# Performance work log

Hardware: AMD Instinct MI355X
Metric: run time of the kernel (lower is better)

Reference implementation:

```python
import jax, jax.numpy as jnp
import numpy as np

SHRINK_THRES = 0.0025
R_THRES = 1.0
EPS = 1e-12


def setup_inputs() -> dict:
    key = jax.random.key(0)
    k1, k2 = jax.random.split(key)
    N, L, D = 16384, 4096, 1024  # samples, memory slots (lan_dim), fea_dim
    x = jax.random.normal(k1, (N, D), dtype=jnp.float32)
    stdv = 1.0 / np.sqrt(D)
    weight = jax.random.uniform(k2, (L, D), dtype=jnp.float32, minval=-stdv, maxval=stdv)
    return {"x": x, "weight": weight}


def reference(x, weight):
    # memory addressing: att = softmax(x @ W^T)  -> [N, L]
    att = jax.nn.softmax(x @ weight.T, axis=1)
    # hard_shrink_relu: relu(a - lambd) * a / (|a - lambd| + eps)
    shifted = att - SHRINK_THRES
    att = jax.nn.relu(shifted) * att / (jnp.abs(shifted) + EPS)
    # L1 normalize along dim 1 (F.normalize p=1, eps=1e-12)
    l1 = jnp.sum(jnp.abs(att), axis=1, keepdims=True)
    att = att / jnp.maximum(l1, EPS)
    # reconstruct from memory: [N, D]
    output = att @ weight
    # nearest landmark per sample (detached gather in original)
    ind = jnp.argmax(att, axis=1)                      # [N]
    nl = weight[ind]                                   # [N, D]
    # second-nearest: overwrite argmax slot with the row minimum, re-argmax
    rows = jnp.arange(att.shape[0])
    row_min = jnp.min(att, axis=1)
    att2 = att.at[rows, ind].set(row_min)
    ind2 = jnp.argmax(att2, axis=1)
    nl2 = weight[ind2]                                 # [N, D]
    # centroid-distance filter (original returns list of indices; we return a
    # jit-compatible boolean mask over samples instead)
    cen = jnp.mean(weight, axis=0)                     # [D]
    dist = jnp.sqrt(jnp.sum((x - cen) ** 2, axis=1))   # [N]
    col_mask = dist < R_THRES                          # [N] bool
    return (output, att, nl, nl2, col_mask)
```

## Files before the change

### kernel.cpp

```cpp
#include <hip/hip_runtime.h>
#include <cmath>

#define NS 16384
#define LS 4096
#define DF 1024
#define SHRINK_T 0.0025f
#define EPS_T 1e-12f

using f16 = _Float16;
using f16x8 = __attribute__((ext_vector_type(8))) _Float16;
using f32x16 = __attribute__((ext_vector_type(16))) float;

#define NSEG 64
#define BM 128
#define BN 128
#define BK 32
#define NKT (DF / BK)

__global__ __launch_bounds__(256) void pack_kernel(
    const float* __restrict__ src, f16* __restrict__ ph, f16* __restrict__ pl)
{
    __shared__ f16 sh[4096];
    __shared__ f16 sl[4096];
    const int t = threadIdx.x;
    const int kt = blockIdx.x;
    const int R = blockIdx.y;
    const int r = t >> 1;
    const int half = t & 1;

    const float* s = src + (size_t)(R * 128 + r) * DF + kt * 32 + half * 16;
    float v[16];
#pragma unroll
    for (int q = 0; q < 4; ++q) {
        float4 f = ((const float4*)s)[q];
        v[q * 4 + 0] = f.x; v[q * 4 + 1] = f.y; v[q * 4 + 2] = f.z; v[q * 4 + 3] = f.w;
    }
    f16 h[16], l[16];
#pragma unroll
    for (int q = 0; q < 16; ++q) {
        h[q] = (f16)v[q];
        l[q] = (f16)(v[q] - (float)h[q]);
    }
    const int j0 = (half * 2) * 1024 + r * 8;
    const int j1 = j0 + 1024;
#pragma unroll
    for (int e = 0; e < 8; ++e) {
        sh[j0 + e] = h[e];     sl[j0 + e] = l[e];
        sh[j1 + e] = h[8 + e]; sl[j1 + e] = l[8 + e];
    }
    __syncthreads();
    const size_t og = ((size_t)R * NKT + kt) * 4096;
    *(f16x8*)&ph[og + t * 8]        = *(const f16x8*)&sh[t * 8];
    *(f16x8*)&ph[og + 2048 + t * 8] = *(const f16x8*)&sh[2048 + t * 8];
    *(f16x8*)&pl[og + t * 8]        = *(const f16x8*)&sl[t * 8];
    *(f16x8*)&pl[og + 2048 + t * 8] = *(const f16x8*)&sl[2048 + t * 8];
}

__global__ void centroid_part_kernel(const float* __restrict__ w, float* __restrict__ part) {
    const int c = blockIdx.x * 256 + threadIdx.x;
    const int seg = blockIdx.y;
    const int l0 = seg * (LS / NSEG);
    float acc = 0.f;
    for (int l = 0; l < LS / NSEG; ++l)
        acc += w[(size_t)(l0 + l) * DF + c];
    part[(size_t)seg * DF + c] = acc;
}

__global__ void centroid_sum_kernel(const float* __restrict__ part, float* __restrict__ cen) {
    const int c = blockIdx.x * 256 + threadIdx.x;
    float acc = 0.f;
    for (int s = 0; s < NSEG; ++s) acc += part[(size_t)s * DF + c];
    cen[c] = acc * (1.0f / (float)LS);
}

#define GLOAD16(gptr, lptr)                                                    \
    __builtin_amdgcn_global_load_lds(                                          \
        (const __attribute__((address_space(1))) void*)(gptr),                 \
        (__attribute__((address_space(3))) void*)(lptr), 16, 0, 0)

__global__ __launch_bounds__(256) void gemm_f16_kernel(
    const f16* __restrict__ xph, const f16* __restrict__ xpl,
    const f16* __restrict__ wph, const f16* __restrict__ wpl,
    float* __restrict__ S, int r0, int rowsChunk)
{
    __shared__ __align__(16) f16 Ah[4096];
    __shared__ __align__(16) f16 Al[4096];
    __shared__ __align__(16) f16 Bh[4096];
    __shared__ __align__(16) f16 Bl[4096];

    const int t = threadIdx.x;
    const int lane = t & 63;
    const int wv = t >> 6;
    const int wr = (wv >> 1) * 64;
    const int wc = (wv & 1) * 64;

    f32x16 acc[2][2];
#pragma unroll
    for (int m = 0; m < 2; ++m)
#pragma unroll
        for (int n = 0; n < 2; ++n)
#pragma unroll
            for (int j = 0; j < 16; ++j) acc[m][n][j] = 0.f;

    const int c32 = lane & 31;
    const int kh = lane >> 5;

    const size_t atile = ((size_t)((r0 >> 7) + blockIdx.y)) * NKT;
    const size_t btile = ((size_t)blockIdx.x) * NKT;
    const int lb0 = wv * 512;
    const int lb1 = 2048 + wv * 512;

#define STAGE(kt)                                                          \
    do {                                                                   \
        const size_t _a = (atile + (kt)) * 4096 + t * 8;                   \
        const size_t _b = (btile + (kt)) * 4096 + t * 8;                   \
        GLOAD16(xph + _a,        &Ah[lb0]);                                \
        GLOAD16(xph + _a + 2048, &Ah[lb1]);                                \
        GLOAD16(xpl + _a,        &Al[lb0]);                                \
        GLOAD16(xpl + _a + 2048, &Al[lb1]);                                \
        GLOAD16(wph + _b,        &Bh[lb0]);                                \
        GLOAD16(wph + _b + 2048, &Bh[lb1]);                                \
        GLOAD16(wpl + _b,        &Bl[lb0]);                                \
        GLOAD16(wpl + _b + 2048, &Bl[lb1]);                                \
    } while (0)

    STAGE(0);

    for (int kt = 0; kt < NKT; ++kt) {
        __syncthreads();

        f16x8 amh[2][2], aml[2][2], bnh[2][2], bnl[2][2];
#pragma unroll
        for (int s = 0; s < 2; ++s) {
            const int pl = s * 2 + kh;
#pragma unroll
            for (int m = 0; m < 2; ++m) {
                const int j = pl * 1024 + (wr + m * 32 + c32) * 8;
                amh[s][m] = *(const f16x8*)&Ah[j];
                aml[s][m] = *(const f16x8*)&Al[j];
            }
#pragma unroll
            for (int n = 0; n < 2; ++n) {
                const int j = pl * 1024 + (wc + n * 32 + c32) * 8;
                bnh[s][n] = *(const f16x8*)&Bh[j];
                bnl[s][n] = *(const f16x8*)&Bl[j];
            }
        }

        __syncthreads();
        if (kt + 1 < NKT) STAGE(kt + 1);

#pragma unroll
        for (int s = 0; s < 2; ++s)
#pragma unroll
            for (int m = 0; m < 2; ++m)
#pragma unroll
                for (int n = 0; n < 2; ++n) {
                    acc[m][n] = __builtin_amdgcn_mfma_f32_32x32x16_f16(amh[s][m], bnh[s][n], acc[m][n], 0, 0, 0);
                    acc[m][n] = __builtin_amdgcn_mfma_f32_32x32x16_f16(amh[s][m], bnl[s][n], acc[m][n], 0, 0, 0);
                    acc[m][n] = __builtin_amdgcn_mfma_f32_32x32x16_f16(aml[s][m], bnh[s][n], acc[m][n], 0, 0, 0);
                }
    }
#undef STAGE

#pragma unroll
    for (int m = 0; m < 2; ++m) {
        const int rb = blockIdx.y * BM + wr + m * 32 + 4 * kh;
#pragma unroll
        for (int n = 0; n < 2; ++n) {
            const int cc = blockIdx.x * BN + wc + n * 32 + c32;
#pragma unroll
            for (int reg = 0; reg < 16; ++reg) {
                const int rr = rb + (reg & 3) + 8 * (reg >> 2);
                if (rr < rowsChunk)
                    S[(size_t)rr * LS + cc] = acc[m][n][reg];
            }
        }
    }
}

__global__ __launch_bounds__(256) void pass2_kernel(
    const float* __restrict__ S, const float* __restrict__ x,
    const float* __restrict__ w, const float* __restrict__ cen,
    float* __restrict__ out, int r0)
{
    constexpr int T = 256;
    __shared__ __align__(16) float att_lds[LS];
    __shared__ float red[T];
    __shared__ int redi[T];

    const int t = threadIdx.x;
    const size_t row = (size_t)r0 + blockIdx.x;
    const float4* s4 = (const float4*)(S + (size_t)blockIdx.x * (size_t)LS);

    float* const out_output = out;
    float* const out_att  = out + (size_t)NS * DF;
    float* const out_nl   = out + (size_t)NS * DF + (size_t)NS * LS;
    float* const out_nl2  = out + (size_t)2 * NS * DF + (size_t)NS * LS;
    float* const out_mask = out + (size_t)3 * NS * DF + (size_t)NS * LS;

    float sv[16];
    float mx = -INFINITY;
#pragma unroll
    for (int i = 0; i < 4; ++i) {
        float4 v = s4[i * 256 + t];
        sv[i * 4 + 0] = v.x; sv[i * 4 + 1] = v.y;
        sv[i * 4 + 2] = v.z; sv[i * 4 + 3] = v.w;
        mx = fmaxf(mx, fmaxf(fmaxf(v.x, v.y), fmaxf(v.z, v.w)));
    }
    red[t] = mx;
    __syncthreads();
    for (int off = 128; off >= 1; off >>= 1) {
        if (t < off) red[t] = fmaxf(red[t], red[t + off]);
        __syncthreads();
    }
    const float m = red[0];
    __syncthreads();

    float zs = 0.f;
#pragma unroll
    for (int i = 0; i < 16; ++i) {
        sv[i] = expf(sv[i] - m);
        zs += sv[i];
    }
    red[t] = zs;
    __syncthreads();
    for (int off = 128; off >= 1; off >>= 1) {
        if (t < off) red[t] += red[t + off];
        __syncthreads();
    }
    const float Z = red[0];
    __syncthreads();

    float l1 = 0.f;
#pragma unroll
    for (int i = 0; i < 16; ++i) {
        float a = sv[i] / Z;
        float r = a - SHRINK_T;
        float v = (r > 0.f) ? (r * a) / (r + EPS_T) : 0.f;
        sv[i] = v;
        l1 += v;
    }
    red[t] = l1;
    __syncthreads();
    for (int off = 128; off >= 1; off >>= 1) {
        if (t < off) red[t] += red[t + off];
        __syncthreads();
    }
    const float nrm = fmaxf(red[0], EPS_T);
    __syncthreads();

    float bv = -INFINITY; int bi = LS;
    float mn = INFINITY;
    float4* const attl4 = (float4*)att_lds;
    float4* const att4o = (float4*)(out_att + row * LS);
#pragma unroll
    for (int i = 0; i < 4; ++i) {
        float4 vn4;
        vn4.x = sv[i * 4 + 0] / nrm; vn4.y = sv[i * 4 + 1] / nrm;
        vn4.z = sv[i * 4 + 2] / nrm; vn4.w = sv[i * 4 + 3] / nrm;
        sv[i * 4 + 0] = vn4.x; sv[i * 4 + 1] = vn4.y;
        sv[i * 4 + 2] = vn4.z; sv[i * 4 + 3] = vn4.w;
        attl4[i * 256 + t] = vn4;
        att4o[i * 256 + t] = vn4;
#pragma unroll
        for (int c = 0; c < 4; ++c) {
            const float v = sv[i * 4 + c];
            const int j = i * 1024 + 4 * t + c;
            if (v > bv) { bv = v; bi = j; }
            mn = fminf(mn, v);
        }
    }
    __syncthreads();

    red[t] = bv; redi[t] = bi;
    __syncthreads();
    for (int off = 128; off >= 1; off >>= 1) {
        if (t < off) {
            float ov = red[t + off]; int oi = redi[t + off];
            if (ov > red[t] || (ov == red[t] && oi < redi[t])) { red[t] = ov; redi[t] = oi; }
        }
        __syncthreads();
    }
    const int ind = redi[0];
    __syncthreads();

    red[t] = mn;
    __syncthreads();
    for (int off = 128; off >= 1; off >>= 1) {
        if (t < off) red[t] = fminf(red[t], red[t + off]);
        __syncthreads();
    }
    const float rowmin = red[0];
    __syncthreads();

    bv = -INFINITY; bi = LS;
#pragma unroll
    for (int i = 0; i < 4; ++i)
#pragma unroll
        for (int c = 0; c < 4; ++c) {
            const int j = i * 1024 + 4 * t + c;
            const float vv = (j == ind) ? rowmin : sv[i * 4 + c];
            if (vv > bv) { bv = vv; bi = j; }
        }
    red[t] = bv; redi[t] = bi;
    __syncthreads();
    for (int off = 128; off >= 1; off >>= 1) {
        if (t < off) {
            float ov = red[t + off]; int oi = redi[t + off];
            if (ov > red[t] || (ov == red[t] && oi < redi[t])) { red[t] = ov; redi[t] = oi; }
        }
        __syncthreads();
    }
    const int ind2 = redi[0];
    __syncthreads();

    const int lane = t & 63;
    float4 oa = {0.f, 0.f, 0.f, 0.f};
    for (int k0 = 0; k0 < LS; k0 += 64) {
        float av = att_lds[k0 + lane];
        unsigned long long msk = __ballot(av > 0.f);
        while (msk) {
            int b = __ffsll((unsigned long long)msk) - 1;
            msk &= msk - 1;
            float vv = att_lds[k0 + b];
            float4 wv4 = ((const float4*)(w + (size_t)(k0 + b) * DF))[t];
            oa.x = fmaf(vv, wv4.x, oa.x);
            oa.y = fmaf(vv, wv4.y, oa.y);
            oa.z = fmaf(vv, wv4.z, oa.z);
            oa.w = fmaf(vv, wv4.w, oa.w);
        }
    }
    ((float4*)(out_output + row * DF))[t] = oa;

    ((float4*)(out_nl  + row * DF))[t] = ((const float4*)(w + (size_t)ind  * DF))[t];
    ((float4*)(out_nl2 + row * DF))[t] = ((const float4*)(w + (size_t)ind2 * DF))[t];

    float4 xv = ((const float4*)(x + row * DF))[t];
    float4 cv = ((const float4*)cen)[t];
    float ds = 0.f;
    ds = fmaf(xv.x - cv.x, xv.x - cv.x, ds);
    ds = fmaf(xv.y - cv.y, xv.y - cv.y, ds);
    ds = fmaf(xv.z - cv.z, xv.z - cv.z, ds);
    ds = fmaf(xv.w - cv.w, xv.w - cv.w, ds);
    red[t] = ds;
    __syncthreads();
    for (int off = 128; off >= 1; off >>= 1) {
        if (t < off) red[t] += red[t + off];
        __syncthreads();
    }
    if (t == 0) {
        float dist = sqrtf(red[0]);
        out_mask[row] = (dist < 1.0f) ? 1.0f : 0.0f;
    }
}

extern "C" void kernel_launch(void* const* d_in, const int* in_sizes, int n_in,
                              void* d_out, int out_size, void* d_ws, size_t ws_size,
                              hipStream_t stream)
{
    const float* x = (const float*)d_in[0];
    const float* w = (const float*)d_in[1];
    float* out = (float*)d_out;

    float* cen = (float*)d_ws;
    float* part = cen + DF;
    f16* xph = (f16*)(part + (size_t)NSEG * DF);
    f16* xpl = xph + (size_t)NS * DF;
    f16* wph = xpl + (size_t)NS * DF;
    f16* wpl = wph + (size_t)LS * DF;
    float* S = (float*)(wpl + (size_t)LS * DF);

    const size_t head_bytes = sizeof(float) * (DF + (size_t)NSEG * DF)
                            + (size_t)2 * 2 * NS * DF + (size_t)2 * 2 * LS * DF;
    long cap_rows = (long)((ws_size - head_bytes) / (sizeof(float) * LS));
    if (cap_rows > NS) cap_rows = NS;
    if (cap_rows < 1) cap_rows = 1;
    int chunk = (cap_rows >= BM) ? (int)(cap_rows - (cap_rows % BM)) : (int)cap_rows;

    centroid_part_kernel<<<dim3(DF / 256, NSEG), 256, 0, stream>>>(w, part);
    centroid_sum_kernel<<<DF / 256, 256, 0, stream>>>(part, cen);
    pack_kernel<<<dim3(NKT, NS / 128), 256, 0, stream>>>(x, xph, xpl);
    pack_kernel<<<dim3(NKT, LS / 128), 256, 0, stream>>>(w, wph, wpl);

    for (int r0 = 0; r0 < NS; r0 += chunk) {
        int rows = (NS - r0 < chunk) ? (NS - r0) : chunk;
        dim3 grid(LS / BN, (rows + BM - 1) / BM);
        gemm_f16_kernel<<<grid, 256, 0, stream>>>(xph, xpl, wph, wpl, S, r0, rows);
        pass2_kernel<<<rows, 256, 0, stream>>>(S, x, w, cen, out, r0);
    }
}
```

Baseline: 558.8 us.

## Double-buffer LDS tiles in split-f16 GEMM with explicit vmcnt waits

Doubles the shared-memory tile buffers in the x·Wᵀ GEMM so the global-to-LDS loads for tile kt+2 are issued while tile kt is consumed. Full __syncthreads are replaced by explicit s_waitcnt vmcnt/lgkmcnt waits and raw s_barrier calls, so only the older prefetch has to land before each step. This hides more global-load latency behind the MFMA work. In exchange LDS use per block doubles to 64KB, which may reduce occupancy, and correctness now depends on hand-counted wait counts.

```diff
diff --git a/kernel.cpp b/kernel.cpp
--- a/kernel.cpp
+++ b/kernel.cpp
@@ -83,10 +83,10 @@
     const f16* __restrict__ wph, const f16* __restrict__ wpl,
     float* __restrict__ S, int r0, int rowsChunk)
 {
-    __shared__ __align__(16) f16 Ah[4096];
-    __shared__ __align__(16) f16 Al[4096];
-    __shared__ __align__(16) f16 Bh[4096];
-    __shared__ __align__(16) f16 Bl[4096];
+    __shared__ __align__(16) f16 Ah[2][4096];
+    __shared__ __align__(16) f16 Al[2][4096];
+    __shared__ __align__(16) f16 Bh[2][4096];
+    __shared__ __align__(16) f16 Bl[2][4096];
 
     const int t = threadIdx.x;
     const int lane = t & 63;
@@ -110,24 +110,30 @@
     const int lb0 = wv * 512;
     const int lb1 = 2048 + wv * 512;
 
-#define STAGE(kt)                                                          \
+#define STAGE(kt, b)                                                       \
     do {                                                                   \
         const size_t _a = (atile + (kt)) * 4096 + t * 8;                   \
         const size_t _b = (btile + (kt)) * 4096 + t * 8;                   \
-        GLOAD16(xph + _a,        &Ah[lb0]);                                \
-        GLOAD16(xph + _a + 2048, &Ah[lb1]);                                \
-        GLOAD16(xpl + _a,        &Al[lb0]);                                \
-        GLOAD16(xpl + _a + 2048, &Al[lb1]);                                \
-        GLOAD16(wph + _b,        &Bh[lb0]);                                \
-        GLOAD16(wph + _b + 2048, &Bh[lb1]);                                \
-        GLOAD16(wpl + _b,        &Bl[lb0]);                                \
-        GLOAD16(wpl + _b + 2048, &Bl[lb1]);                                \
+        GLOAD16(xph + _a,        &Ah[b][lb0]);                             \
+        GLOAD16(xph + _a + 2048, &Ah[b][lb1]);                             \
+        GLOAD16(xpl + _a,        &Al[b][lb0]);                             \
+        GLOAD16(xpl + _a + 2048, &Al[b][lb1]);                             \
+        GLOAD16(wph + _b,        &Bh[b][lb0]);                             \
+        GLOAD16(wph + _b + 2048, &Bh[b][lb1]);                             \
+        GLOAD16(wpl + _b,        &Bl[b][lb0]);                             \
+        GLOAD16(wpl + _b + 2048, &Bl[b][lb1]);                             \
     } while (0)
 
-    STAGE(0);
+    STAGE(0, 0);
+    STAGE(1, 1);
 
     for (int kt = 0; kt < NKT; ++kt) {
-        __syncthreads();
+        const int b = kt & 1;
+        if (kt == NKT - 1) asm volatile("s_waitcnt vmcnt(0)" ::: "memory");
+        else               asm volatile("s_waitcnt vmcnt(8)" ::: "memory");
+        __builtin_amdgcn_sched_barrier(0);
+        __builtin_amdgcn_s_barrier();
+        __builtin_amdgcn_sched_barrier(0);
 
         f16x8 amh[2][2], aml[2][2], bnh[2][2], bnl[2][2];
 #pragma unroll
@@ -136,19 +142,21 @@
 #pragma unroll
             for (int m = 0; m < 2; ++m) {
                 const int j = pl * 1024 + (wr + m * 32 + c32) * 8;
-                amh[s][m] = *(const f16x8*)&Ah[j];
-                aml[s][m] = *(const f16x8*)&Al[j];
+                amh[s][m] = *(const f16x8*)&Ah[b][j];
+                aml[s][m] = *(const f16x8*)&Al[b][j];
             }
 #pragma unroll
             for (int n = 0; n < 2; ++n) {
                 const int j = pl * 1024 + (wc + n * 32 + c32) * 8;
-                bnh[s][n] = *(const f16x8*)&Bh[j];
-                bnl[s][n] = *(const f16x8*)&Bl[j];
+                bnh[s][n] = *(const f16x8*)&Bh[b][j];
+                bnl[s][n] = *(const f16x8*)&Bl[b][j];
             }
         }
-
-        __syncthreads();
-        if (kt + 1 < NKT) STAGE(kt + 1);
+        asm volatile("s_waitcnt lgkmcnt(0)" ::: "memory");
+        __builtin_amdgcn_sched_barrier(0);
+        __builtin_amdgcn_s_barrier();
+
+        if (kt + 2 < NKT) STAGE(kt + 2, b);
 
 #pragma unroll
         for (int s = 0; s < 2; ++s)
```

New measurement: 571.3 us. 2.2% more time.
